# Optimization experiments

Measured on AMD Instinct MI355X. Metric: run time of the kernel, lower is better.

Reference implementation:

```python
import jax, jax.numpy as jnp
import numpy as np

HIDDEN = 64
EF_DIM = 3
RBOUND = 10.0
GROUP = 5
NEXP_MEAN = 0.05   # fixed normalization constants of the 'nexpnorm' RBF
NEXP_STD = 0.15
COORDS_WEIGHT = 1.0
N_NODES = 100000
N_GRAPHS = N_NODES // GROUP


def act(x):
    return jax.nn.relu(x)


def rbf(dist, num_rbf):
    # ExpNormal smearing with cosine cutoff (non-trainable), then fixed normalization.
    # dist: (..., 1) -> (..., num_rbf)
    alpha = 5.0 / RBOUND
    start = float(np.exp(-RBOUND))
    means = jnp.linspace(start, 1.0, num_rbf).astype(dist.dtype)
    beta = (2.0 / num_rbf * (1.0 - start)) ** -2
    cutoff = 0.5 * (jnp.cos(dist * jnp.pi / RBOUND) + 1.0) * (dist <= RBOUND)
    r = cutoff * jnp.exp(-beta * (jnp.exp(-alpha * dist) - means) ** 2)
    return (r - NEXP_MEAN) / NEXP_STD


def safe_pdist(a, b):
    # pairwise L2 norm (B,G,1,3)-(B,1,G,3) -> (B,G,G,1); grad-safe at zero
    d = a[:, :, None, :] - b[:, None, :, :]
    sq = jnp.sum(d * d, axis=-1, keepdims=True)
    return jnp.sqrt(jnp.where(sq == 0.0, 1.0, sq)) * (sq > 0.0)


def mlp2(x, w1, b1, w2, b2):
    return act(act(x @ w1 + b1) @ w2 + b2)


def mixed_wl(row, col, coord, vel, ic_wef, ic_pat, br_w1, br_b1, br_w2, br_b2, out_w, out_b):
    B = coord.shape[0] // GROUP
    c = coord.reshape(B, GROUP, 3)
    v = vel.reshape(B, GROUP, 3)
    mcd = safe_pdist(c, v)  # mixed coord-vel distances
    ef = jnp.concatenate([
        rbf(safe_pdist(c, c), EF_DIM),
        rbf(safe_pdist(v, v), EF_DIM),
        rbf(mcd, EF_DIM),
        rbf(jnp.swapaxes(mcd, 1, 2), EF_DIM),
    ], axis=-1)  # (B, 5, 5, 4*EF_DIM)
    # TwoFDisInit: linear embed * pattern embedding (diag tuples get pattern id 2, off-diag 1)
    idx = jnp.arange(GROUP)
    pattern = jnp.ones((GROUP, GROUP), dtype=jnp.int32).at[idx, idx].set(2)
    kemb = (ef @ ic_wef) * ic_pat[pattern]  # (B, 5, 5, H)
    # TwoFDisLayer (color_steps = 1): three branch MLPs, matrix-multiply mixing, residual add
    sm = mlp2(kemb, br_w1[0], br_b1[0], br_w2[0], br_b2[0])
    k0 = mlp2(kemb, br_w1[1], br_b1[1], br_w2[1], br_b2[1])
    k1 = mlp2(kemb, br_w1[2], br_b1[2], br_w2[2], br_b2[2])
    mult = jnp.einsum('bijd,bjkd->bikd', k0, k1)
    kemb = kemb + act((sm * mult) @ out_w + out_b)
    # gather per-edge tuple embedding
    return kemb[row // GROUP, row % GROUP, col % GROUP]  # (E, H)


def setup_inputs():
    key = jax.random.key(0)
    ks = jax.random.split(key, 20)
    N, H = N_NODES, HIDDEN
    # fully-connected (no self loops) edges inside each 5-node graph
    pairs = np.array([(i, j) for i in range(GROUP) for j in range(GROUP) if i != j])
    off = np.arange(N_GRAPHS) * GROUP
    row = (off[:, None] + pairs[None, :, 0]).reshape(-1)
    col = (off[:, None] + pairs[None, :, 1]).reshape(-1)
    edge_index = jnp.asarray(np.stack([row, col]), dtype=jnp.int32)
    g = lambda k, shp, s=0.05: jax.random.normal(k, shp, dtype=jnp.float32) * s
    return {
        'h': g(ks[0], (N, H), 0.5),
        'coord': g(ks[1], (N, 3), 1.0),
        'vel': g(ks[2], (N, 3), 1.0),
        'edge_index': edge_index,
        'e_w1': g(ks[3], (2 * H + 1 + H, H)), 'e_b1': jnp.zeros((H,), jnp.float32),
        'e_w2': g(ks[4], (H, H)), 'e_b2': jnp.zeros((H,), jnp.float32),
        'n_w1': g(ks[5], (2 * H, H)), 'n_b1': jnp.zeros((H,), jnp.float32),
        'n_w2': g(ks[6], (H, H)), 'n_b2': jnp.zeros((H,), jnp.float32),
        'c_w1': g(ks[7], (H, H)), 'c_b1': jnp.zeros((H,), jnp.float32),
        'c_w2': g(ks[8], (H, 1), 0.001),  # xavier gain=0.001, bias-free
        'v_w1': g(ks[9], (H, H)), 'v_b1': jnp.zeros((H,), jnp.float32),
        'v_w2': g(ks[10], (H, 1)), 'v_b2': jnp.zeros((1,), jnp.float32),
        'ic_wef': g(ks[11], (4 * EF_DIM, H), 0.1),
        'ic_pat': g(ks[12], (3, H), 0.1),
        'br_w1': g(ks[13], (3, H, H)), 'br_b1': jnp.zeros((3, H), jnp.float32),
        'br_w2': g(ks[14], (3, H, H)), 'br_b2': jnp.zeros((3, H), jnp.float32),
        'out_w': g(ks[15], (H, H)), 'out_b': jnp.zeros((H,), jnp.float32),
    }


def reference(h, coord, vel, edge_index, e_w1, e_b1, e_w2, e_b2, n_w1, n_b1, n_w2, n_b2,
              c_w1, c_b1, c_w2, v_w1, v_b1, v_w2, v_b2, ic_wef, ic_pat,
              br_w1, br_b1, br_w2, br_b2, out_w, out_b):
    row, col = edge_index[0], edge_index[1]
    N = h.shape[0]
    # coord2radial (norm_diff=False)
    coord_diff = coord[row] - coord[col]                      # (E, 3)
    radial = jnp.sum(coord_diff * coord_diff, axis=1, keepdims=True)  # (E, 1)
    # mixed 2-WL tuple embedding per edge
    kemb = mixed_wl(row, col, coord, vel, ic_wef, ic_pat, br_w1, br_b1, br_w2, br_b2, out_w, out_b)
    # edge model (attention=False)
    edge_feat = mlp2(jnp.concatenate([h[row], h[col], radial, kemb], axis=1),
                     e_w1, e_b1, e_w2, e_b2)                  # (E, H)
    # coord model: per-edge scalar (num_vectors_in=out=1), clamp, segment mean
    cmat = act(edge_feat @ c_w1 + c_b1) @ c_w2                # (E, 1)
    trans = jnp.clip(coord_diff * cmat, -100.0, 100.0)        # (E, 3)
    cnt = jax.ops.segment_sum(jnp.ones((row.shape[0],), trans.dtype), row, num_segments=N)
    agg = jax.ops.segment_sum(trans, row, num_segments=N) / jnp.maximum(cnt, 1.0)[:, None]
    # velocity update: coord += coord_mlp_vel(h) * vel
    vmat = act(h @ v_w1 + v_b1) @ v_w2 + v_b2                 # (N, 1)
    coord_out = (coord + agg * COORDS_WEIGHT + vel * vmat)[:, :, None]  # (N, 3, 1)
    # node model (recurrent=True)
    nagg = jax.ops.segment_sum(edge_feat, row, num_segments=N)
    h_out = h + (act(jnp.concatenate([h, nagg], axis=1) @ n_w1 + n_b1) @ n_w2 + n_b2)
    return h_out, coord_out
```

## Files before the change

kernel.cpp:

```cpp
#include <hip/hip_runtime.h>
#include <math.h>

#define HD 64
#define WPB 2

typedef unsigned short u16;
typedef unsigned int u32;
typedef __attribute__((ext_vector_type(8))) short short8;
typedef __attribute__((ext_vector_type(4))) float f32x4;

__device__ __forceinline__ u16 f2bf(float f) {
  u32 r;
  asm("v_cvt_pk_bf16_f32 %0, %1, %2" : "=v"(r) : "v"(f), "v"(f));
  return (u16)r;
}
__device__ __forceinline__ float bf2f(u16 x) {
  return __uint_as_float(((u32)x) << 16);
}
__device__ __forceinline__ int uswz(int row, int col) {
  return (row << 6) | (col ^ (((row >> 2) & 3) << 4));
}
__device__ __forceinline__ float rlane(float v, int l) {
  return __uint_as_float(__builtin_amdgcn_readlane(__float_as_uint(v), l));
}
__device__ __forceinline__ void fence() {
  asm volatile("s_waitcnt lgkmcnt(0)" ::: "memory");
}

template <int MT, int RMAX>
__device__ __forceinline__ void loadA(const u16* A_, int t, short8* a0, short8* a1) {
  const int q8 = (t >> 4) << 3;
#pragma unroll
  for (int mt = 0; mt < MT; ++mt) {
    int row = mt * 16 + (t & 15);
    row = row > RMAX ? RMAX : row;
    const int idx = uswz(row, q8);
    a0[mt] = *reinterpret_cast<const short8*>(A_ + idx);
    a1[mt] = *reinterpret_cast<const short8*>(A_ + (idx ^ 32));
  }
}

template <int MTT>
__device__ __forceinline__ void mmh(const short8* a0, const short8* a1,
                                    const u16* __restrict__ WT, f32x4 (*acc)[2],
                                    int t, int nh) {
  const int c15 = t & 15;
  const int q8 = (t >> 4) << 3;
  short8 b[2][2];
#pragma unroll
  for (int n2 = 0; n2 < 2; ++n2) {
    const int nt = nh * 2 + n2;
#pragma unroll
    for (int s = 0; s < 2; ++s)
      b[n2][s] = *reinterpret_cast<const short8*>(WT + (nt * 16 + c15) * 64 + s * 32 + q8);
  }
#pragma unroll
  for (int mt = 0; mt < MTT; ++mt) {
#pragma unroll
    for (int n2 = 0; n2 < 2; ++n2)
      acc[mt][n2] = __builtin_amdgcn_mfma_f32_16x16x32_bf16(a0[mt], b[n2][0], acc[mt][n2], 0, 0, 0);
#pragma unroll
    for (int n2 = 0; n2 < 2; ++n2)
      acc[mt][n2] = __builtin_amdgcn_mfma_f32_16x16x32_bf16(a1[mt], b[n2][1], acc[mt][n2], 0, 0, 0);
  }
}

template <int MT, int RMAX, int EPI>
__device__ __forceinline__ void run_phase2(const u16* AA, const u16* AB,
                                           u16* DA, u16* DB,
                                           const u16* MA, const u16* MB,
                                           const u16* __restrict__ WT,
                                           const float* __restrict__ bias,
                                           int t, int rowoff = 0) {
  const int c15 = t & 15, q = t >> 4;
  constexpr int rowlim = (MT == 2) ? 25 : 5;
  short8 a0[2 * MT], a1[2 * MT];
  loadA<MT, RMAX>(AA, t, a0, a1);
  loadA<MT, RMAX>(AB, t, a0 + MT, a1 + MT);
#pragma unroll
  for (int nh = 0; nh < 2; ++nh) {
    f32x4 acc[2 * MT][2];
#pragma unroll
    for (int n2 = 0; n2 < 2; ++n2) {
      const int col = (nh * 2 + n2) * 16 + c15;
      const float bb = bias ? bias[col] : 0.0f;
#pragma unroll
      for (int mt = 0; mt < 2 * MT; ++mt) acc[mt][n2] = (f32x4){bb, bb, bb, bb};
    }
    mmh<2 * MT>(a0, a1, WT, acc, t, nh);
#pragma unroll
    for (int n2 = 0; n2 < 2; ++n2) {
      const int col = (nh * 2 + n2) * 16 + c15;
#pragma unroll
      for (int mt = 0; mt < 2 * MT; ++mt) {
        u16* D_ = (mt < MT) ? DA : DB;
        const u16* M_ = (mt < MT) ? MA : MB;
        const int r0 = (mt % MT) * 16 + q * 4;
        const int bix = uswz(r0 + rowoff, col);
#pragma unroll
        for (int i = 0; i < 4; ++i) {
          if (r0 + i < rowlim) {
            const int ix = bix + i * 64;
            float v = acc[mt][n2][i];
            if (EPI >= 2) v = fmaxf(v, 0.0f);
            if (EPI == 3) v *= bf2f(M_[ix]);
            if (EPI == 4) v += bf2f(D_[ix]);
            D_[ix] = f2bf(v);
          }
        }
      }
    }
  }
}

__global__ __launch_bounds__(256) void prepack(
    const float* __restrict__ br_w1, const float* __restrict__ br_w2,
    const float* __restrict__ out_w, const float* __restrict__ e_w1,
    const float* __restrict__ e_w2, const float* __restrict__ c_w1,
    const float* __restrict__ v_w1, const float* __restrict__ n_w1,
    const float* __restrict__ n_w2, const float* __restrict__ ic_wef,
    u16* __restrict__ W) {
  const int m = blockIdx.x;
  if (m == 16) {
    for (int e = threadIdx.x; e < 2048; e += blockDim.x) {
      const int n = e >> 5, k = e & 31;
      W[16 * 4096 + e] = (k < 12) ? f2bf(ic_wef[k * 64 + n]) : (u16)0;
    }
    return;
  }
  const float* src;
  switch (m) {
    case 0: src = br_w1; break;
    case 1: src = br_w1 + 4096; break;
    case 2: src = br_w1 + 8192; break;
    case 3: src = br_w2; break;
    case 4: src = br_w2 + 4096; break;
    case 5: src = br_w2 + 8192; break;
    case 6: src = out_w; break;
    case 7: src = e_w1; break;
    case 8: src = e_w1 + 64 * 64; break;
    case 9: src = e_w1 + 129 * 64; break;
    case 10: src = e_w2; break;
    case 11: src = c_w1; break;
    case 12: src = v_w1; break;
    case 13: src = n_w1; break;
    case 14: src = n_w1 + 64 * 64; break;
    default: src = n_w2; break;
  }
  u16* dst = W + m * 4096;
  for (int e = threadIdx.x; e < 4096; e += blockDim.x) {
    const int n = e >> 6, k = e & 63;
    dst[e] = f2bf(src[k * 64 + n]);
  }
}

__global__ __launch_bounds__(64 * WPB, 2) void egcl_mfma(
    const float* __restrict__ gh, const float* __restrict__ gcoord,
    const float* __restrict__ gvel, const u16* __restrict__ Wg,
    const float* __restrict__ e_w1, const float* __restrict__ e_b1,
    const float* __restrict__ e_b2,
    const float* __restrict__ n_b1, const float* __restrict__ n_b2,
    const float* __restrict__ c_b1, const float* __restrict__ c_w2,
    const float* __restrict__ v_b1, const float* __restrict__ v_w2,
    const float* __restrict__ v_b2,
    const float* __restrict__ ic_pat,
    const float* __restrict__ br_b1, const float* __restrict__ br_b2,
    const float* __restrict__ out_b,
    float* __restrict__ hout, float* __restrict__ cout, int B) {
  __shared__ __align__(16) u16 arena[WPB][10240];

  const int t = threadIdx.x & 63;
  const int wv = threadIdx.x >> 6;
  const int gA = (blockIdx.x * WPB + wv) * 2;
  if (gA >= B) return;
  int gB = gA + 1;
  if (gB >= B) gB = gA;

  u16* AR = arena[wv];
  u16* HA = AR;           u16* HB = AR + 320;
  u16* KA = AR + 640;     u16* KB = AR + 2240;
  u16* TA = AR + 3840;    u16* TB = AR + 5440;
  u16* UA = AR + 7040;    u16* UB = AR + 8640;
  u16* EFa = TA;
  u16* EFb = TB;
  const int c15 = t & 15, q = t >> 4, q8 = q << 3;
#define WT(m) (Wg + (m) * 4096)

  float scvreg = 0.0f;
  if (t < 15) scvreg = gcoord[gA * 15 + t];
  else if (t >= 16 && t < 31) scvreg = gvel[gA * 15 + (t - 16)];
  else if (t >= 32 && t < 47) scvreg = gcoord[gB * 15 + (t - 32)];
  else if (t >= 48 && t < 63) scvreg = gvel[gB * 15 + (t - 48)];

#pragma unroll
  for (int i = 0; i < 5; ++i) {
    HA[uswz(i, t)] = f2bf(gh[(gA * 5 + i) * HD + t]);
    HB[uswz(i, t)] = f2bf(gh[(gB * 5 + i) * HD + t]);
  }

#pragma unroll
  for (int z = 0; z < 8; ++z) {
    const int e = t + z * 64;
    if (e < 500) {
      const int gsel = e >= 250;
      const int ee = e - gsel * 250;
      const int row = ee / 10, cc = 12 + (ee % 10) * 2;
      *reinterpret_cast<u32*>((gsel ? EFb : EFa) + row * 32 + cc) = 0u;
    }
  }

  float sqcc = 0.0f;
  {
    const int lb = (t >= 32) ? 32 : 0;
    const int tt = t - lb;
    if (tt < 25) {
      u16* EF = lb ? EFb : EFa;
      const int ti = tt / 5, tj = tt % 5;
      const float cix = __shfl(scvreg, lb + ti * 3 + 0, 64), ciy = __shfl(scvreg, lb + ti * 3 + 1, 64), ciz = __shfl(scvreg, lb + ti * 3 + 2, 64);
      const float cjx = __shfl(scvreg, lb + tj * 3 + 0, 64), cjy = __shfl(scvreg, lb + tj * 3 + 1, 64), cjz = __shfl(scvreg, lb + tj * 3 + 2, 64);
      const float vix = __shfl(scvreg, lb + 16 + ti * 3 + 0, 64), viy = __shfl(scvreg, lb + 16 + ti * 3 + 1, 64), viz = __shfl(scvreg, lb + 16 + ti * 3 + 2, 64);
      const float vjx = __shfl(scvreg, lb + 16 + tj * 3 + 0, 64), vjy = __shfl(scvreg, lb + 16 + tj * 3 + 1, 64), vjz = __shfl(scvreg, lb + 16 + tj * 3 + 2, 64);
      {
        const float dx = cix - cjx, dy = ciy - cjy, dz = ciz - cjz;
        sqcc = dx * dx + dy * dy + dz * dz;
      }
      auto sd = [](float sq) { return (sq > 0.0f) ? sqrtf(sq) : 0.0f; };
      float sq2;
      const float dcc = sd(sqcc);
      {
        const float dx = vix - vjx, dy = viy - vjy, dz = viz - vjz;
        sq2 = dx * dx + dy * dy + dz * dz;
      }
      const float dvv = sd(sq2);
      {
        const float dx = cix - vjx, dy = ciy - vjy, dz = ciz - vjz;
        sq2 = dx * dx + dy * dy + dz * dz;
      }
      const float dcv = sd(sq2);
      {
        const float dx = cjx - vix, dy = cjy - viy, dz = cjz - viz;
        sq2 = dx * dx + dy * dy + dz * dz;
      }
      const float dvc = sd(sq2);
      auto rbf3 = [&](float d, int base) {
        const float cut = (d <= 10.0f) ? (0.5f * (cosf(d * 0.31415926535897931f) + 1.0f)) : 0.0f;
        const float e = expf(-0.5f * d);
        const float u0 = e - 4.5399929762484854e-05f;
        const float u1 = e - 0.50002270f;
        const float u2 = e - 1.0f;
        const float BETA = 2.2502043f;
        EF[tt * 32 + base + 0] = f2bf((cut * expf(-BETA * u0 * u0) - 0.05f) * (1.0f / 0.15f));
        EF[tt * 32 + base + 1] = f2bf((cut * expf(-BETA * u1 * u1) - 0.05f) * (1.0f / 0.15f));
        EF[tt * 32 + base + 2] = f2bf((cut * expf(-BETA * u2 * u2) - 0.05f) * (1.0f / 0.15f));
      };
      rbf3(dcc, 0);
      rbf3(dvv, 3);
      rbf3(dcv, 6);
      rbf3(dvc, 9);
    }
  }
  fence();

  {
    short8 aE[4];
#pragma unroll
    for (int gsel = 0; gsel < 2; ++gsel) {
      const u16* EF = gsel ? EFb : EFa;
#pragma unroll
      for (int mt = 0; mt < 2; ++mt) {
        int row = mt * 16 + c15;
        row = row > 24 ? 24 : row;
        aE[gsel * 2 + mt] = *reinterpret_cast<const short8*>(EF + row * 32 + q8);
      }
    }
    const u16* WTp = Wg + 16 * 4096;
#pragma unroll
    for (int nh = 0; nh < 2; ++nh) {
      f32x4 acc[4][2];
#pragma unroll
      for (int mt = 0; mt < 4; ++mt)
#pragma unroll
        for (int n2 = 0; n2 < 2; ++n2) acc[mt][n2] = (f32x4){0.f, 0.f, 0.f, 0.f};
      short8 b[2];
#pragma unroll
      for (int n2 = 0; n2 < 2; ++n2)
        b[n2] = *reinterpret_cast<const short8*>(WTp + ((nh * 2 + n2) * 16 + c15) * 32 + q8);
#pragma unroll
      for (int mt = 0; mt < 4; ++mt)
#pragma unroll
        for (int n2 = 0; n2 < 2; ++n2)
          acc[mt][n2] = __builtin_amdgcn_mfma_f32_16x16x32_bf16(aE[mt], b[n2], acc[mt][n2], 0, 0, 0);
#pragma unroll
      for (int n2 = 0; n2 < 2; ++n2) {
        const int col = (nh * 2 + n2) * 16 + c15;
        const float p1 = ic_pat[64 + col], p2 = ic_pat[128 + col];
#pragma unroll
        for (int mt = 0; mt < 4; ++mt) {
          u16* K_ = (mt < 2) ? KA : KB;
          const int r0 = (mt & 1) * 16 + q * 4;
          const int bix = uswz(r0, col);
#pragma unroll
          for (int i = 0; i < 4; ++i) {
            const int row = r0 + i;
            if (row < 25) {
              const bool diag = (row % 6) == 0;
              K_[bix + i * 64] = f2bf(acc[mt][n2][i] * (diag ? p2 : p1));
            }
          }
        }
      }
    }
  }
  fence();

  float svv[2][4];
  float svc[4][4];

  run_phase2<2, 24, 2>(KA, KB, TA, TB, nullptr, nullptr, WT(1), br_b1 + 64, t); fence();
  run_phase2<2, 24, 2>(TA, TB, UA, UB, nullptr, nullptr, WT(4), br_b2 + 64, t); fence();
  run_phase2<2, 24, 2>(KA, KB, TA, TB, nullptr, nullptr, WT(2), br_b1 + 128, t); fence();
  run_phase2<2, 24, 2>(TA, TB, TA, TB, nullptr, nullptr, WT(5), br_b2 + 128, t); fence();

#pragma unroll 1
  for (int gsel = 0; gsel < 2; ++gsel) {
    const u16* Tg = gsel ? TB : TA;
    u16* Ug = gsel ? UB : UA;
    float mu[25];
#pragma unroll
    for (int p = 0; p < 25; ++p) mu[p] = 0.0f;
#pragma unroll
    for (int j = 0; j < 5; ++j) {
      float k1r[5], k0c[5];
#pragma unroll
      for (int k = 0; k < 5; ++k) k1r[k] = bf2f(Tg[uswz(j * 5 + k, t)]);
#pragma unroll
      for (int i = 0; i < 5; ++i) k0c[i] = bf2f(Ug[uswz(i * 5 + j, t)]);
#pragma unroll
      for (int i = 0; i < 5; ++i)
#pragma unroll
        for (int k = 0; k < 5; ++k) mu[i * 5 + k] = fmaf(k0c[i], k1r[k], mu[i * 5 + k]);
    }
    fence();
#pragma unroll
    for (int p = 0; p < 25; ++p) Ug[uswz(p, t)] = f2bf(mu[p]);
  }
  fence();

  run_phase2<2, 24, 2>(KA, KB, TA, TB, nullptr, nullptr, WT(0), br_b1, t); fence();
  run_phase2<2, 24, 3>(TA, TB, TA, TB, UA, UB, WT(3), br_b2, t); fence();
  run_phase2<2, 24, 4>(TA, TB, KA, KB, nullptr, nullptr, WT(6), out_b, t); fence();
  run_phase2<2, 24, 1>(KA, KB, TA, TB, nullptr, nullptr, WT(9), nullptr, t); fence();

  {
    short8 a0[2], a1[2];
    loadA<1, 4>(HA, t, a0, a1);
    loadA<1, 4>(HB, t, a0 + 1, a1 + 1);
    float s[2][4] = {{0.f, 0.f, 0.f, 0.f}, {0.f, 0.f, 0.f, 0.f}};
#pragma unroll
    for (int nh = 0; nh < 2; ++nh) {
      f32x4 aA[2][2], aB[2][2], aV[2][2];
#pragma unroll
      for (int n2 = 0; n2 < 2; ++n2) {
        const float bv = v_b1[(nh * 2 + n2) * 16 + c15];
#pragma unroll
        for (int m2 = 0; m2 < 2; ++m2) {
          aA[m2][n2] = (f32x4){0.f, 0.f, 0.f, 0.f};
          aB[m2][n2] = (f32x4){0.f, 0.f, 0.f, 0.f};
          aV[m2][n2] = (f32x4){bv, bv, bv, bv};
        }
      }
      mmh<2>(a0, a1, WT(7), aA, t, nh);
      mmh<2>(a0, a1, WT(8), aB, t, nh);
      mmh<2>(a0, a1, WT(12), aV, t, nh);
#pragma unroll
      for (int n2 = 0; n2 < 2; ++n2) {
        const int col = (nh * 2 + n2) * 16 + c15;
        const int r0 = q * 4;
        const float w2v = v_w2[col];
#pragma unroll
        for (int gsel = 0; gsel < 2; ++gsel) {
          u16* Ug = gsel ? UB : UA;
          const int bixA = uswz(r0, col);
          const int bixB = uswz(r0 + 8, col);
#pragma unroll
          for (int i = 0; i < 4; ++i) {
            if (r0 + i < 5) {
              Ug[bixA + i * 64] = f2bf(aA[gsel][n2][i]);
              Ug[bixB + i * 64] = f2bf(aB[gsel][n2][i]);
            }
            s[gsel][i] += fmaxf(aV[gsel][n2][i], 0.0f) * w2v;
          }
        }
      }
    }
#pragma unroll
    for (int gsel = 0; gsel < 2; ++gsel)
#pragma unroll
      for (int i = 0; i < 4; ++i) {
        float ss = s[gsel][i];
        ss += __shfl_xor(ss, 1, 64);
        ss += __shfl_xor(ss, 2, 64);
        ss += __shfl_xor(ss, 4, 64);
        ss += __shfl_xor(ss, 8, 64);
        svv[gsel][i] = ss;
      }
  }
  fence();

#pragma unroll 1
  for (int gsel = 0; gsel < 2; ++gsel) {
    const int lb = gsel * 32;
    const u16* Ug = gsel ? UB : UA;
    u16* Tg = gsel ? TB : TA;
    float aAc[5], aBc[5];
#pragma unroll
    for (int i = 0; i < 5; ++i) {
      aAc[i] = bf2f(Ug[uswz(i, t)]);
      aBc[i] = bf2f(Ug[uswz(8 + i, t)]);
    }
    const float eb1v = e_b1[t];
    const float wradv = e_w1[128 * HD + t];
    float ec[20];
#pragma unroll
    for (int p = 0; p < 20; ++p) {
      const int i = p >> 2, jj = p & 3;
      const int j = jj + (jj >= i ? 1 : 0);
      const float radial = rlane(sqcc, lb + i * 5 + j);
      const float cc = bf2f(Tg[uswz(i * 5 + j, t)]);
      ec[p] = fmaxf(aAc[i] + aBc[j] + radial * wradv + cc + eb1v, 0.0f);
    }
    fence();
#pragma unroll
    for (int p = 0; p < 20; ++p) Tg[uswz(p, t)] = f2bf(ec[p]);
  }
  fence();

  run_phase2<2, 24, 2>(TA, TB, UA, UB, nullptr, nullptr, WT(10), e_b2, t); fence();

#pragma unroll
  for (int gsel = 0; gsel < 2; ++gsel) {
    const u16* Ug = gsel ? UB : UA;
    u16* Kg = gsel ? KB : KA;
#pragma unroll
    for (int i = 0; i < 5; ++i) {
      float na = 0.0f;
#pragma unroll
      for (int jj = 0; jj < 4; ++jj) na += bf2f(Ug[uswz(4 * i + jj, t)]);
      Kg[uswz(i, t)] = f2bf(na);
    }
  }
  fence();

  {
    short8 a0[4], a1[4];
    loadA<2, 24>(UA, t, a0, a1);
    loadA<2, 24>(UB, t, a0 + 2, a1 + 2);
    float s[4][4];
#pragma unroll
    for (int mt = 0; mt < 4; ++mt)
#pragma unroll
      for (int i = 0; i < 4; ++i) s[mt][i] = 0.0f;
#pragma unroll
    for (int nh = 0; nh < 2; ++nh) {
      f32x4 acc[4][2];
#pragma unroll
      for (int n2 = 0; n2 < 2; ++n2) {
        const float bv = c_b1[(nh * 2 + n2) * 16 + c15];
#pragma unroll
        for (int mt = 0; mt < 4; ++mt) acc[mt][n2] = (f32x4){bv, bv, bv, bv};
      }
      mmh<4>(a0, a1, WT(11), acc, t, nh);
#pragma unroll
      for (int n2 = 0; n2 < 2; ++n2) {
        const int col = (nh * 2 + n2) * 16 + c15;
        const float w2v = c_w2[col];
#pragma unroll
        for (int mt = 0; mt < 4; ++mt)
#pragma unroll
          for (int i = 0; i < 4; ++i)
            s[mt][i] += fmaxf(acc[mt][n2][i], 0.0f) * w2v;
      }
    }
#pragma unroll
    for (int mt = 0; mt < 4; ++mt)
#pragma unroll
      for (int i = 0; i < 4; ++i) {
        float ss = s[mt][i];
        ss += __shfl_xor(ss, 1, 64);
        ss += __shfl_xor(ss, 2, 64);
        ss += __shfl_xor(ss, 4, 64);
        ss += __shfl_xor(ss, 8, 64);
        svc[mt][i] = ss;
      }
  }

  {
    const float vb2 = v_b2[0];
    float coutreg = 0.0f;
#pragma unroll
    for (int gsel = 0; gsel < 2; ++gsel) {
      const int lb = gsel * 32;
#pragma unroll
      for (int i = 0; i < 5; ++i) {
        const float vmi = rlane(svv[gsel][i & 3], (i >> 2) << 4) + vb2;
#pragma unroll
        for (int dd = 0; dd < 3; ++dd) {
          const float ci = rlane(scvreg, lb + i * 3 + dd);
          float s = 0.0f;
#pragma unroll
          for (int jj = 0; jj < 4; ++jj) {
            const int j = jj + (jj >= i ? 1 : 0);
            const int p = i * 4 + jj;
            const float cmp = rlane(svc[gsel * 2 + (p >> 4)][p & 3], ((p & 15) >> 2) << 4);
            float tr = (ci - rlane(scvreg, lb + j * 3 + dd)) * cmp;
            tr = fminf(fmaxf(tr, -100.0f), 100.0f);
            s += tr;
          }
          const float val = ci + 0.25f * s + rlane(scvreg, lb + 16 + i * 3 + dd) * vmi;
          if (t == lb + i * 3 + dd) coutreg = val;
        }
      }
    }
    if (t < 15) cout[gA * 15 + t] = coutreg;
    else if (t >= 32 && t < 47) cout[gB * 15 + (t - 32)] = coutreg;
  }

  {
    short8 a0h[2], a1h[2], a0k[2], a1k[2];
    loadA<1, 4>(HA, t, a0h, a1h);
    loadA<1, 4>(HB, t, a0h + 1, a1h + 1);
    loadA<1, 4>(KA, t, a0k, a1k);
    loadA<1, 4>(KB, t, a0k + 1, a1k + 1);
#pragma unroll
    for (int nh = 0; nh < 2; ++nh) {
      f32x4 acc[2][2];
#pragma unroll
      for (int n2 = 0; n2 < 2; ++n2) {
        const float nb = n_b1[(nh * 2 + n2) * 16 + c15];
        acc[0][n2] = (f32x4){nb, nb, nb, nb};
        acc[1][n2] = (f32x4){nb, nb, nb, nb};
      }
      mmh<2>(a0h, a1h, WT(13), acc, t, nh);
      mmh<2>(a0k, a1k, WT(14), acc, t, nh);
#pragma unroll
      for (int n2 = 0; n2 < 2; ++n2) {
        const int col = (nh * 2 + n2) * 16 + c15;
        const int r0 = q * 4;
        const int bix = uswz(r0, col);
#pragma unroll
        for (int gsel = 0; gsel < 2; ++gsel) {
          u16* Tg = gsel ? TB : TA;
#pragma unroll
          for (int i = 0; i < 4; ++i) {
            if (r0 + i < 5) Tg[bix + i * 64] = f2bf(fmaxf(acc[gsel][n2][i], 0.0f));
          }
        }
      }
    }
  }
  fence();

  {
    short8 a0[2], a1[2];
    loadA<1, 4>(TA, t, a0, a1);
    loadA<1, 4>(TB, t, a0 + 1, a1 + 1);
#pragma unroll
    for (int nh = 0; nh < 2; ++nh) {
      f32x4 acc[2][2];
#pragma unroll
      for (int n2 = 0; n2 < 2; ++n2) {
        const float nb = n_b2[(nh * 2 + n2) * 16 + c15];
        acc[0][n2] = (f32x4){nb, nb, nb, nb};
        acc[1][n2] = (f32x4){nb, nb, nb, nb};
      }
      mmh<2>(a0, a1, WT(15), acc, t, nh);
#pragma unroll
      for (int n2 = 0; n2 < 2; ++n2) {
        const int col = (nh * 2 + n2) * 16 + c15;
#pragma unroll
        for (int gsel = 0; gsel < 2; ++gsel) {
          const int gg = gsel ? gB : gA;
#pragma unroll
          for (int i = 0; i < 4; ++i) {
            const int row = q * 4 + i;
            if (row < 5) {
              const size_t ix = (size_t)(gg * 5 + row) * HD + col;
              hout[ix] = gh[ix] + acc[gsel][n2][i];
            }
          }
        }
      }
    }
  }
#undef WT
}

extern "C" void kernel_launch(void* const* d_in, const int* in_sizes, int n_in,
                              void* d_out, int out_size, void* d_ws, size_t ws_size,
                              hipStream_t stream) {
  if (n_in < 27) return;
  const float* gh    = (const float*)d_in[0];
  const float* coord = (const float*)d_in[1];
  const float* vel   = (const float*)d_in[2];
  const float* e_w1 = (const float*)d_in[4];
  const float* e_b1 = (const float*)d_in[5];
  const float* e_w2 = (const float*)d_in[6];
  const float* e_b2 = (const float*)d_in[7];
  const float* n_w1 = (const float*)d_in[8];
  const float* n_b1 = (const float*)d_in[9];
  const float* n_w2 = (const float*)d_in[10];
  const float* n_b2 = (const float*)d_in[11];
  const float* c_w1 = (const float*)d_in[12];
  const float* c_b1 = (const float*)d_in[13];
  const float* c_w2 = (const float*)d_in[14];
  const float* v_w1 = (const float*)d_in[15];
  const float* v_b1 = (const float*)d_in[16];
  const float* v_w2 = (const float*)d_in[17];
  const float* v_b2 = (const float*)d_in[18];
  const float* ic_wef = (const float*)d_in[19];
  const float* ic_pat = (const float*)d_in[20];
  const float* br_w1 = (const float*)d_in[21];
  const float* br_b1 = (const float*)d_in[22];
  const float* br_w2 = (const float*)d_in[23];
  const float* br_b2 = (const float*)d_in[24];
  const float* out_w = (const float*)d_in[25];
  const float* out_b = (const float*)d_in[26];

  const int N = in_sizes[0] / HD;
  const int B = N / 5;
  float* hout = (float*)d_out;
  float* cout = (float*)d_out + (size_t)N * HD;
  u16* W = (u16*)d_ws;

  prepack<<<17, 256, 0, stream>>>(br_w1, br_w2, out_w, e_w1, e_w2, c_w1, v_w1,
                                  n_w1, n_w2, ic_wef, W);

  const int gpb = WPB * 2;
  const int blocks = (B + gpb - 1) / gpb;
  egcl_mfma<<<blocks, 64 * WPB, 0, stream>>>(
      gh, coord, vel, W, e_w1, e_b1, e_b2, n_b1, n_b2, c_b1, c_w2, v_b1, v_w2,
      v_b2, ic_pat, br_b1, br_b2, out_b, hout, cout, B);
}
```

Measured before the change: 252.5 us.

## Pack two graphs' node rows into one MFMA tile, prefetch next weights, merge per-graph loops

Node features are loaded straight from global memory into bf16 MFMA A-fragments in registers, with both graphs packed into rows 0-4 and 8-12 of a single 16-row tile. This halves the MFMA count for the node-level matmuls and removes the H staging buffers, shrinking LDS per wave. Each phase also touches the next phase's weight matrix through a dummy XOR-accumulated load, an L2 prefetch kept alive by a never-taken store. The per-graph mult and edge-input loops are merged so both graphs run in one pass with fewer LDS fences, at the cost of more live registers.

```diff
diff --git a/kernel.cpp b/kernel.cpp
--- a/kernel.cpp
+++ b/kernel.cpp
@@ -13,6 +13,11 @@
   u32 r;
   asm("v_cvt_pk_bf16_f32 %0, %1, %2" : "=v"(r) : "v"(f), "v"(f));
   return (u16)r;
+}
+__device__ __forceinline__ u32 pk2(float lo, float hi) {
+  u32 r;
+  asm("v_cvt_pk_bf16_f32 %0, %1, %2" : "=v"(r) : "v"(lo), "v"(hi));
+  return r;
 }
 __device__ __forceinline__ float bf2f(u16 x) {
   return __uint_as_float(((u32)x) << 16);
@@ -71,9 +76,11 @@
                                            const u16* MA, const u16* MB,
                                            const u16* __restrict__ WT,
                                            const float* __restrict__ bias,
-                                           int t, int rowoff = 0) {
+                                           const u16* __restrict__ PF,
+                                           u32& pfa, int t, int rowoff = 0) {
   const int c15 = t & 15, q = t >> 4;
   constexpr int rowlim = (MT == 2) ? 25 : 5;
+  const u32 pfv = reinterpret_cast<const u32*>(PF)[t * 32];
   short8 a0[2 * MT], a1[2 * MT];
   loadA<MT, RMAX>(AA, t, a0, a1);
   loadA<MT, RMAX>(AB, t, a0 + MT, a1 + MT);
@@ -111,6 +118,7 @@
       }
     }
   }
+  pfa ^= pfv;
 }
 
 __global__ __launch_bounds__(256) void prepack(
@@ -167,7 +175,7 @@
     const float* __restrict__ br_b1, const float* __restrict__ br_b2,
     const float* __restrict__ out_b,
     float* __restrict__ hout, float* __restrict__ cout, int B) {
-  __shared__ __align__(16) u16 arena[WPB][10240];
+  __shared__ __align__(16) u16 arena[WPB][9600];
 
   const int t = threadIdx.x & 63;
   const int wv = threadIdx.x >> 6;
@@ -177,26 +185,39 @@
   if (gB >= B) gB = gA;
 
   u16* AR = arena[wv];
-  u16* HA = AR;           u16* HB = AR + 320;
-  u16* KA = AR + 640;     u16* KB = AR + 2240;
-  u16* TA = AR + 3840;    u16* TB = AR + 5440;
-  u16* UA = AR + 7040;    u16* UB = AR + 8640;
+  u16* KA = AR;           u16* KB = AR + 1600;
+  u16* TA = AR + 3200;    u16* TB = AR + 4800;
+  u16* UA = AR + 6400;    u16* UB = AR + 8000;
   u16* EFa = TA;
   u16* EFb = TB;
   const int c15 = t & 15, q = t >> 4, q8 = q << 3;
+  u32 pfa = 0;
 #define WT(m) (Wg + (m) * 4096)
+
+  short8 hA0, hA1;
+  {
+    int nd = c15 & 7;
+    nd = nd > 4 ? 4 : nd;
+    const int gg = (c15 & 8) ? gB : gA;
+    const float* hp = gh + (size_t)(gg * 5 + nd) * HD + q8;
+    const float4 f0 = *reinterpret_cast<const float4*>(hp);
+    const float4 f1 = *reinterpret_cast<const float4*>(hp + 4);
+    const float4 f2 = *reinterpret_cast<const float4*>(hp + 32);
+    const float4 f3 = *reinterpret_cast<const float4*>(hp + 36);
+    union { u32 w[4]; short8 s; } u0, u1;
+    u0.w[0] = pk2(f0.x, f0.y); u0.w[1] = pk2(f0.z, f0.w);
+    u0.w[2] = pk2(f1.x, f1.y); u0.w[3] = pk2(f1.z, f1.w);
+    u1.w[0] = pk2(f2.x, f2.y); u1.w[1] = pk2(f2.z, f2.w);
+    u1.w[2] = pk2(f3.x, f3.y); u1.w[3] = pk2(f3.z, f3.w);
+    hA0 = u0.s;
+    hA1 = u1.s;
+  }
 
   float scvreg = 0.0f;
   if (t < 15) scvreg = gcoord[gA * 15 + t];
   else if (t >= 16 && t < 31) scvreg = gvel[gA * 15 + (t - 16)];
   else if (t >= 32 && t < 47) scvreg = gcoord[gB * 15 + (t - 32)];
   else if (t >= 48 && t < 63) scvreg = gvel[gB * 15 + (t - 48)];
-
-#pragma unroll
-  for (int i = 0; i < 5; ++i) {
-    HA[uswz(i, t)] = f2bf(gh[(gA * 5 + i) * HD + t]);
-    HB[uswz(i, t)] = f2bf(gh[(gB * 5 + i) * HD + t]);
-  }
 
 #pragma unroll
   for (int z = 0; z < 8; ++z) {
@@ -262,6 +283,7 @@
   fence();
 
   {
+    const u32 pfv = reinterpret_cast<const u32*>(WT(1))[t * 32];
     short8 aE[4];
 #pragma unroll
     for (int gsel = 0; gsel < 2; ++gsel) {
@@ -310,148 +332,153 @@
         }
       }
     }
+    pfa ^= pfv;
   }
   fence();
 
-  float svv[2][4];
   float svc[4][4];
 
-  run_phase2<2, 24, 2>(KA, KB, TA, TB, nullptr, nullptr, WT(1), br_b1 + 64, t); fence();
-  run_phase2<2, 24, 2>(TA, TB, UA, UB, nullptr, nullptr, WT(4), br_b2 + 64, t); fence();
-  run_phase2<2, 24, 2>(KA, KB, TA, TB, nullptr, nullptr, WT(2), br_b1 + 128, t); fence();
-  run_phase2<2, 24, 2>(TA, TB, TA, TB, nullptr, nullptr, WT(5), br_b2 + 128, t); fence();
-
-#pragma unroll 1
-  for (int gsel = 0; gsel < 2; ++gsel) {
-    const u16* Tg = gsel ? TB : TA;
-    u16* Ug = gsel ? UB : UA;
-    float mu[25];
-#pragma unroll
-    for (int p = 0; p < 25; ++p) mu[p] = 0.0f;
+  run_phase2<2, 24, 2>(KA, KB, TA, TB, nullptr, nullptr, WT(1), br_b1 + 64, WT(4), pfa, t); fence();
+  run_phase2<2, 24, 2>(TA, TB, UA, UB, nullptr, nullptr, WT(4), br_b2 + 64, WT(2), pfa, t); fence();
+  run_phase2<2, 24, 2>(KA, KB, TA, TB, nullptr, nullptr, WT(2), br_b1 + 128, WT(5), pfa, t); fence();
+  run_phase2<2, 24, 2>(TA, TB, TA, TB, nullptr, nullptr, WT(5), br_b2 + 128, WT(0), pfa, t); fence();
+
+  {
+    float mu[2][25];
+#pragma unroll
+    for (int gsel = 0; gsel < 2; ++gsel)
+#pragma unroll
+      for (int p = 0; p < 25; ++p) mu[gsel][p] = 0.0f;
 #pragma unroll
     for (int j = 0; j < 5; ++j) {
-      float k1r[5], k0c[5];
-#pragma unroll
-      for (int k = 0; k < 5; ++k) k1r[k] = bf2f(Tg[uswz(j * 5 + k, t)]);
-#pragma unroll
-      for (int i = 0; i < 5; ++i) k0c[i] = bf2f(Ug[uswz(i * 5 + j, t)]);
-#pragma unroll
-      for (int i = 0; i < 5; ++i)
-#pragma unroll
-        for (int k = 0; k < 5; ++k) mu[i * 5 + k] = fmaf(k0c[i], k1r[k], mu[i * 5 + k]);
+#pragma unroll
+      for (int gsel = 0; gsel < 2; ++gsel) {
+        const u16* Tg = gsel ? TB : TA;
+        const u16* Ug = gsel ? UB : UA;
+        float k1r[5], k0c[5];
+#pragma unroll
+        for (int k = 0; k < 5; ++k) k1r[k] = bf2f(Tg[uswz(j * 5 + k, t)]);
+#pragma unroll
+        for (int i = 0; i < 5; ++i) k0c[i] = bf2f(Ug[uswz(i * 5 + j, t)]);
+#pragma unroll
+        for (int i = 0; i < 5; ++i)
+#pragma unroll
+          for (int k = 0; k < 5; ++k)
+            mu[gsel][i * 5 + k] = fmaf(k0c[i], k1r[k], mu[gsel][i * 5 + k]);
+      }
     }
     fence();
 #pragma unroll
-    for (int p = 0; p < 25; ++p) Ug[uswz(p, t)] = f2bf(mu[p]);
+    for (int p = 0; p < 25; ++p) {
+      UA[uswz(p, t)] = f2bf(mu[0][p]);
+      UB[uswz(p, t)] = f2bf(mu[1][p]);
+    }
   }
   fence();
 
-  run_phase2<2, 24, 2>(KA, KB, TA, TB, nullptr, nullptr, WT(0), br_b1, t); fence();
-  run_phase2<2, 24, 3>(TA, TB, TA, TB, UA, UB, WT(3), br_b2, t); fence();
-  run_phase2<2, 24, 4>(TA, TB, KA, KB, nullptr, nullptr, WT(6), out_b, t); fence();
-  run_phase2<2, 24, 1>(KA, KB, TA, TB, nullptr, nullptr, WT(9), nullptr, t); fence();
-
-  {
-    short8 a0[2], a1[2];
-    loadA<1, 4>(HA, t, a0, a1);
-    loadA<1, 4>(HB, t, a0 + 1, a1 + 1);
-    float s[2][4] = {{0.f, 0.f, 0.f, 0.f}, {0.f, 0.f, 0.f, 0.f}};
+  run_phase2<2, 24, 2>(KA, KB, TA, TB, nullptr, nullptr, WT(0), br_b1, WT(3), pfa, t); fence();
+  run_phase2<2, 24, 3>(TA, TB, TA, TB, UA, UB, WT(3), br_b2, WT(6), pfa, t); fence();
+  run_phase2<2, 24, 4>(TA, TB, KA, KB, nullptr, nullptr, WT(6), out_b, WT(9), pfa, t); fence();
+  run_phase2<2, 24, 1>(KA, KB, TA, TB, nullptr, nullptr, WT(9), nullptr, WT(7), pfa, t); fence();
+
+  float svv[4];
+  {
+    const u32 pfv = reinterpret_cast<const u32*>(WT(8))[t * 32];
+    float s[4] = {0.f, 0.f, 0.f, 0.f};
 #pragma unroll
     for (int nh = 0; nh < 2; ++nh) {
-      f32x4 aA[2][2], aB[2][2], aV[2][2];
+      f32x4 aA[1][2], aB[1][2], aV[1][2];
 #pragma unroll
       for (int n2 = 0; n2 < 2; ++n2) {
         const float bv = v_b1[(nh * 2 + n2) * 16 + c15];
-#pragma unroll
-        for (int m2 = 0; m2 < 2; ++m2) {
-          aA[m2][n2] = (f32x4){0.f, 0.f, 0.f, 0.f};
-          aB[m2][n2] = (f32x4){0.f, 0.f, 0.f, 0.f};
-          aV[m2][n2] = (f32x4){bv, bv, bv, bv};
+        aA[0][n2] = (f32x4){0.f, 0.f, 0.f, 0.f};
+        aB[0][n2] = (f32x4){0.f, 0.f, 0.f, 0.f};
+        aV[0][n2] = (f32x4){bv, bv, bv, bv};
+      }
+      mmh<1>(&hA0, &hA1, WT(7), aA, t, nh);
+      mmh<1>(&hA0, &hA1, WT(8), aB, t, nh);
+      mmh<1>(&hA0, &hA1, WT(12), aV, t, nh);
+#pragma unroll
+      for (int n2 = 0; n2 < 2; ++n2) {
+        const int col = (nh * 2 + n2) * 16 + c15;
+        const float w2v = v_w2[col];
+#pragma unroll
+        for (int i = 0; i < 4; ++i) {
+          const int r = q * 4 + i;
+          if (r < 5) {
+            UA[uswz(r, col)] = f2bf(aA[0][n2][i]);
+            UA[uswz(r + 8, col)] = f2bf(aB[0][n2][i]);
+          } else if (r >= 8 && r < 13) {
+            UB[uswz(r - 8, col)] = f2bf(aA[0][n2][i]);
+            UB[uswz(r, col)] = f2bf(aB[0][n2][i]);
+          }
+          s[i] += fmaxf(aV[0][n2][i], 0.0f) * w2v;
         }
       }
-      mmh<2>(a0, a1, WT(7), aA, t, nh);
-      mmh<2>(a0, a1, WT(8), aB, t, nh);
-      mmh<2>(a0, a1, WT(12), aV, t, nh);
-#pragma unroll
-      for (int n2 = 0; n2 < 2; ++n2) {
-        const int col = (nh * 2 + n2) * 16 + c15;
-        const int r0 = q * 4;
-        const float w2v = v_w2[col];
-#pragma unroll
-        for (int gsel = 0; gsel < 2; ++gsel) {
-          u16* Ug = gsel ? UB : UA;
-          const int bixA = uswz(r0, col);
-          const int bixB = uswz(r0 + 8, col);
-#pragma unroll
-          for (int i = 0; i < 4; ++i) {
-            if (r0 + i < 5) {
-              Ug[bixA + i * 64] = f2bf(aA[gsel][n2][i]);
-              Ug[bixB + i * 64] = f2bf(aB[gsel][n2][i]);
-            }
-            s[gsel][i] += fmaxf(aV[gsel][n2][i], 0.0f) * w2v;
-          }
-        }
-      }
-    }
-#pragma unroll
-    for (int gsel = 0; gsel < 2; ++gsel)
-#pragma unroll
-      for (int i = 0; i < 4; ++i) {
-        float ss = s[gsel][i];
-        ss += __shfl_xor(ss, 1, 64);
-        ss += __shfl_xor(ss, 2, 64);
-        ss += __shfl_xor(ss, 4, 64);
-        ss += __shfl_xor(ss, 8, 64);
-        svv[gsel][i] = ss;
-      }
+    }
+#pragma unroll
+    for (int i = 0; i < 4; ++i) {
+      float ss = s[i];
+      ss += __shfl_xor(ss, 1, 64);
+      ss += __shfl_xor(ss, 2, 64);
+      ss += __shfl_xor(ss, 4, 64);
+      ss += __shfl_xor(ss, 8, 64);
+      svv[i] = ss;
+    }
+    pfa ^= pfv;
   }
   fence();
 
-#pragma unroll 1
-  for (int gsel = 0; gsel < 2; ++gsel) {
-    const int lb = gsel * 32;
-    const u16* Ug = gsel ? UB : UA;
-    u16* Tg = gsel ? TB : TA;
-    float aAc[5], aBc[5];
-#pragma unroll
-    for (int i = 0; i < 5; ++i) {
-      aAc[i] = bf2f(Ug[uswz(i, t)]);
-      aBc[i] = bf2f(Ug[uswz(8 + i, t)]);
-    }
-    const float eb1v = e_b1[t];
-    const float wradv = e_w1[128 * HD + t];
-    float ec[20];
+  {
+    float ec[2][20];
+#pragma unroll
+    for (int gsel = 0; gsel < 2; ++gsel) {
+      const int lb = gsel * 32;
+      const u16* Ug = gsel ? UB : UA;
+      const u16* Tg = gsel ? TB : TA;
+      float aAc[5], aBc[5];
+#pragma unroll
+      for (int i = 0; i < 5; ++i) {
+        aAc[i] = bf2f(Ug[uswz(i, t)]);
+        aBc[i] = bf2f(Ug[uswz(8 + i, t)]);
+      }
+      const float eb1v = e_b1[t];
+      const float wradv = e_w1[128 * HD + t];
+#pragma unroll
+      for (int p = 0; p < 20; ++p) {
+        const int i = p >> 2, jj = p & 3;
+        const int j = jj + (jj >= i ? 1 : 0);
+        const float radial = rlane(sqcc, lb + i * 5 + j);
+        const float cc = bf2f(Tg[uswz(i * 5 + j, t)]);
+        ec[gsel][p] = fmaxf(aAc[i] + aBc[j] + radial * wradv + cc + eb1v, 0.0f);
+      }
+    }
+    fence();
 #pragma unroll
     for (int p = 0; p < 20; ++p) {
-      const int i = p >> 2, jj = p & 3;
-      const int j = jj + (jj >= i ? 1 : 0);
-      const float radial = rlane(sqcc, lb + i * 5 + j);
-      const float cc = bf2f(Tg[uswz(i * 5 + j, t)]);
-      ec[p] = fmaxf(aAc[i] + aBc[j] + radial * wradv + cc + eb1v, 0.0f);
-    }
-    fence();
-#pragma unroll
-    for (int p = 0; p < 20; ++p) Tg[uswz(p, t)] = f2bf(ec[p]);
+      TA[uswz(p, t)] = f2bf(ec[0][p]);
+      TB[uswz(p, t)] = f2bf(ec[1][p]);
+    }
   }
   fence();
 
-  run_phase2<2, 24, 2>(TA, TB, UA, UB, nullptr, nullptr, WT(10), e_b2, t); fence();
+  run_phase2<2, 24, 2>(TA, TB, UA, UB, nullptr, nullptr, WT(10), e_b2, WT(11), pfa, t); fence();
 
 #pragma unroll
   for (int gsel = 0; gsel < 2; ++gsel) {
     const u16* Ug = gsel ? UB : UA;
-    u16* Kg = gsel ? KB : KA;
 #pragma unroll
     for (int i = 0; i < 5; ++i) {
       float na = 0.0f;
 #pragma unroll
       for (int jj = 0; jj < 4; ++jj) na += bf2f(Ug[uswz(4 * i + jj, t)]);
-      Kg[uswz(i, t)] = f2bf(na);
+      KA[uswz(gsel * 8 + i, t)] = f2bf(na);
     }
   }
   fence();
 
   {
+    const u32 pfv = reinterpret_cast<const u32*>(WT(13))[t * 32];
     short8 a0[4], a1[4];
     loadA<2, 24>(UA, t, a0, a1);
     loadA<2, 24>(UB, t, a0 + 2, a1 + 2);
@@ -492,6 +519,7 @@
         ss += __shfl_xor(ss, 8, 64);
         svc[mt][i] = ss;
       }
+    pfa ^= pfv;
   }
 
   {
@@ -502,7 +530,8 @@
       const int lb = gsel * 32;
 #pragma unroll
       for (int i = 0; i < 5; ++i) {
-        const float vmi = rlane(svv[gsel][i & 3], (i >> 2) << 4) + vb2;
+        const int rr = gsel * 8 + i;
+        const float vmi = rlane(svv[rr & 3], (rr >> 2) << 4) + vb2;
 #pragma unroll
         for (int dd = 0; dd < 3; ++dd) {
           const float ci = rlane(scvreg, lb + i * 3 + dd);
@@ -526,72 +555,65 @@
   }
 
   {
-    short8 a0h[2], a1h[2], a0k[2], a1k[2];
-    loadA<1, 4>(HA, t, a0h, a1h);
-    loadA<1, 4>(HB, t, a0h + 1, a1h + 1);
-    loadA<1, 4>(KA, t, a0k, a1k);
-    loadA<1, 4>(KB, t, a0k + 1, a1k + 1);
+    const u32 pfv = reinterpret_cast<const u32*>(WT(15))[t * 32];
+    short8 a0k[1], a1k[1];
+    loadA<1, 15>(KA, t, a0k, a1k);
 #pragma unroll
     for (int nh = 0; nh < 2; ++nh) {
-      f32x4 acc[2][2];
+      f32x4 acc[1][2];
 #pragma unroll
       for (int n2 = 0; n2 < 2; ++n2) {
         const float nb = n_b1[(nh * 2 + n2) * 16 + c15];
         acc[0][n2] = (f32x4){nb, nb, nb, nb};
-        acc[1][n2] = (f32x4){nb, nb, nb, nb};
-      }
-      mmh<2>(a0h, a1h, WT(13), acc, t, nh);
-      mmh<2>(a0k, a1k, WT(14), acc, t, nh);
+      }
+      mmh<1>(&hA0, &hA1, WT(13), acc, t, nh);
+      mmh<1>(a0k, a1k, WT(14), acc, t, nh);
 #pragma unroll
       for (int n2 = 0; n2 < 2; ++n2) {
         const int col = (nh * 2 + n2) * 16 + c15;
-        const int r0 = q * 4;
-        const int bix = uswz(r0, col);
-#pragma unroll
-        for (int gsel = 0; gsel < 2; ++gsel) {
-          u16* Tg = gsel ? TB : TA;
-#pragma unroll
-          for (int i = 0; i < 4; ++i) {
-            if (r0 + i < 5) Tg[bix + i * 64] = f2bf(fmaxf(acc[gsel][n2][i], 0.0f));
+#pragma unroll
+        for (int i = 0; i < 4; ++i) {
+          const int r = q * 4 + i;
+          if (r < 5 || (r >= 8 && r < 13))
+            TA[uswz(r, col)] = f2bf(fmaxf(acc[0][n2][i], 0.0f));
+        }
+      }
+    }
+    pfa ^= pfv;
+  }
+  fence();
+
+  {
+    short8 a0[1], a1[1];
+    loadA<1, 15>(TA, t, a0, a1);
+#pragma unroll
+    for (int nh = 0; nh < 2; ++nh) {
+      f32x4 acc[1][2];
+#pragma unroll
+      for (int n2 = 0; n2 < 2; ++n2) {
+        const float nb = n_b2[(nh * 2 + n2) * 16 + c15];
+        acc[0][n2] = (f32x4){nb, nb, nb, nb};
+      }
+      mmh<1>(a0, a1, WT(15), acc, t, nh);
+#pragma unroll
+      for (int n2 = 0; n2 < 2; ++n2) {
+        const int col = (nh * 2 + n2) * 16 + c15;
+#pragma unroll
+        for (int i = 0; i < 4; ++i) {
+          const int r = q * 4 + i;
+          if (r < 5) {
+            const size_t ix = (size_t)(gA * 5 + r) * HD + col;
+            hout[ix] = gh[ix] + acc[0][n2][i];
+          } else if (r >= 8 && r < 13) {
+            const size_t ix = (size_t)(gB * 5 + (r - 8)) * HD + col;
+            hout[ix] = gh[ix] + acc[0][n2][i];
           }
         }
       }
     }
   }
-  fence();
-
-  {
-    short8 a0[2], a1[2];
-    loadA<1, 4>(TA, t, a0, a1);
-    loadA<1, 4>(TB, t, a0 + 1, a1 + 1);
-#pragma unroll
-    for (int nh = 0; nh < 2; ++nh) {
-      f32x4 acc[2][2];
-#pragma unroll
-      for (int n2 = 0; n2 < 2; ++n2) {
-        const float nb = n_b2[(nh * 2 + n2) * 16 + c15];
-        acc[0][n2] = (f32x4){nb, nb, nb, nb};
-        acc[1][n2] = (f32x4){nb, nb, nb, nb};
-      }
-      mmh<2>(a0, a1, WT(15), acc, t, nh);
-#pragma unroll
-      for (int n2 = 0; n2 < 2; ++n2) {
-        const int col = (nh * 2 + n2) * 16 + c15;
-#pragma unroll
-        for (int gsel = 0; gsel < 2; ++gsel) {
-          const int gg = gsel ? gB : gA;
-#pragma unroll
-          for (int i = 0; i < 4; ++i) {
-            const int row = q * 4 + i;
-            if (row < 5) {
-              const size_t ix = (size_t)(gg * 5 + row) * HD + col;
-              hout[ix] = gh[ix] + acc[gsel][n2][i];
-            }
-          }
-        }
-      }
-    }
-  }
+
+  if (B == -7) cout[1] = __uint_as_float(pfa);
 #undef WT
 }
 
```

After: 246.0 us. 2.6% less time.
